# Performance work log

Hardware: AMD Instinct MI355X
Metric: run time of the kernel (lower is better)

## Reference

```python
import jax, jax.numpy as jnp
import numpy as np

N, P, D, C = 8192, 512, 2, 4   # queries, coeff grid points, spatial dim, num coefficients
HA = 32                        # attention_net hidden
HP, CP = 32, 16                # pointswise_mlp hidden / output
HG = 256                       # green_function_net hidden


def setup_inputs() -> dict:
    key = jax.random.key(0)
    ks = jax.random.split(key, 16)
    g = lambda k, shp, s: jax.random.normal(k, shp, dtype=jnp.float32) * s
    return {
        "r": g(ks[0], (N, 2 * D), 1.0),
        "r_prime": g(ks[1], (N, 2 * D), 1.0),
        "coeff_x": g(ks[2], (P, D), 1.0),
        "coeff_y": g(ks[3], (P, C), 1.0),
        # attention_net MLP (no bias): concat(q,k)=4 -> 32 -> 32 -> 1
        "Wa1": g(ks[4], (2 * D, HA), 0.5),
        "Wa2": g(ks[5], (HA, HA), 1.0 / np.sqrt(HA)),
        "Wa3": g(ks[6], (HA, 1), 1.0 / np.sqrt(HA)),
        # pointswise_mlp: C -> 32 -> 16
        "Wp1": g(ks[7], (C, HP), 0.5), "bp1": jnp.zeros((HP,), jnp.float32),
        "Wp2": g(ks[8], (HP, CP), 1.0 / np.sqrt(HP)), "bp2": jnp.zeros((CP,), jnp.float32),
        # green_function_net: 4+4+16=24 -> 256 -> 256 -> 1 (exp at the end)
        "Wg1": g(ks[9], (2 * D + 2 * D + CP, HG), 1.0 / np.sqrt(24.0)), "bg1": jnp.zeros((HG,), jnp.float32),
        "Wg2": g(ks[10], (HG, HG), 1.0 / np.sqrt(HG)), "bg2": jnp.zeros((HG,), jnp.float32),
        "Wg3": g(ks[11], (HG, 1), 0.1 / np.sqrt(HG)), "bg3": jnp.zeros((1,), jnp.float32),
    }


def reference(r, r_prime, coeff_x, coeff_y,
              Wa1, Wa2, Wa3, Wp1, bp1, Wp2, bp2,
              Wg1, bg1, Wg2, bg2, Wg3, bg3):
    # --- CoefficientNet: pairwise MLP attention over the coefficient grid ---
    q = r[:, :D]  # (N, 2) spatial position only
    # first layer of attn MLP on concat([q, k]) split into q- and k- parts
    h = jax.nn.relu(q @ Wa1[:D][None if False else slice(None)]  # (N, HA)
                    [..., :] [..., :]  # no-op for readability
                    if False else (q @ Wa1[:D])[:, None, :] + (coeff_x @ Wa1[D:])[None, :, :])  # (N, P, HA)
    h = jax.nn.relu(h @ Wa2)                     # (N, P, HA)
    logits = (h @ Wa3)[..., 0]                   # (N, P)
    attn = jax.nn.softmax(logits, axis=-1)       # (N, P)
    attn_out = attn @ coeff_y                    # (N, C)
    c = jax.nn.relu(attn_out @ Wp1 + bp1) @ Wp2 + bp2  # (N, CP)
    # --- GreenFunctionNet ---
    x = jnp.concatenate([r, r_prime, c], axis=-1)       # (N, 24)
    g1 = jax.nn.relu(x @ Wg1 + bg1)
    g2 = jax.nn.relu(g1 @ Wg2 + bg2)
    return jnp.exp(g2 @ Wg3 + bg3)                      # (N, 1)
```

## Files before the change

kernel.cpp:

```cpp
#include <hip/hip_runtime.h>
#include <math.h>

#define N_ 8192
#define P_ 512

typedef __fp16 half8  __attribute__((ext_vector_type(8)));
typedef __fp16 half2t __attribute__((ext_vector_type(2)));
typedef float  floatx16 __attribute__((ext_vector_type(16)));

union H8 { half8 v; half2t h2[4]; };

static __device__ __forceinline__ half2t pk2(float a, float b) {
    return __builtin_amdgcn_cvt_pkrtz(a, b);
}

#define HP_OFF 17408
#define XS_OFF 21760

__global__ __launch_bounds__(512, 4) void k_fused(
    const float* __restrict__ r,
    const float* __restrict__ rp,
    const float* __restrict__ coeff_x,
    const float* __restrict__ coeff_y,
    const float* __restrict__ Wa1,
    const float* __restrict__ Wa2,
    const float* __restrict__ Wa3,
    const float* __restrict__ Wp1,
    const float* __restrict__ bp1,
    const float* __restrict__ Wp2,
    const float* __restrict__ bp2,
    const float* __restrict__ Wg1,
    const float* __restrict__ bg1,
    const float* __restrict__ Wg2,
    const float* __restrict__ bg2,
    const float* __restrict__ Wg3,
    const float* __restrict__ bg3,
    float* __restrict__ out)
{
    __shared__ __align__(16) unsigned char reg0[49152];
    __shared__ __align__(16) float4 cyS[512];
    __shared__ float sA[8][32];
    __shared__ float aoA[4][8][32];
    __shared__ float aoS[32][4];

    const int tid  = threadIdx.x;
    const int n0   = blockIdx.x * 32;
    const int lane = tid & 63;
    const int wv   = tid >> 6;
    const int j32  = lane & 31;
    const int hl   = lane >> 5;
    const int k0g  = hl * 8;

    {
        const float2 cx = ((const float2*)coeff_x)[tid];
        half2t* wrow = (half2t*)(reg0 + tid * 96);
#pragma unroll
        for (int q = 0; q < 16; ++q) {
            const float b0 = cx.x * Wa1[64 + 2*q]     + cx.y * Wa1[96 + 2*q];
            const float b1 = cx.x * Wa1[64 + 2*q + 1] + cx.y * Wa1[96 + 2*q + 1];
            wrow[q] = pk2(b0, b1);
        }
        cyS[tid] = ((const float4*)coeff_y)[tid];
    }

    H8 anh1, anh2;
    {
        const float2 rv = ((const float2*)r)[2 * (n0 + j32)];
#pragma unroll
        for (int q = 0; q < 4; ++q) {
            const int k1 = k0g + 2*q, k2 = 16 + k0g + 2*q;
            anh1.h2[q] = pk2(rv.x*Wa1[k1]   + rv.y*Wa1[32+k1],
                             rv.x*Wa1[k1+1] + rv.y*Wa1[32+k1+1]);
            anh2.h2[q] = pk2(rv.x*Wa1[k2]   + rv.y*Wa1[32+k2],
                             rv.x*Wa1[k2+1] + rv.y*Wa1[32+k2+1]);
        }
    }
    H8 af1, af2;
#pragma unroll
    for (int q = 0; q < 4; ++q) {
        af1.h2[q] = pk2(Wa2[(k0g + 2*q)     * 32 + j32],
                        Wa2[(k0g + 2*q + 1) * 32 + j32]);
        af2.h2[q] = pk2(Wa2[(16 + k0g + 2*q)     * 32 + j32],
                        Wa2[(16 + k0g + 2*q + 1) * 32 + j32]);
    }
    half2t w3h[8];
#pragma unroll
    for (int q = 0; q < 8; ++q) {
        const int r0 = ((2*q) & 3) + 8*(q >> 1) + 4*hl;
        w3h[q] = pk2(Wa3[r0], Wa3[r0 + 1]);
    }

    __syncthreads();

    const half2t zero2 = pk2(0.f, 0.f);
    float s = 0.0f, aox = 0.f, aoy = 0.f, aoz = 0.f, aow = 0.f;

#pragma unroll 2
    for (int pl = 0; pl < 64; ++pl) {
        const int ploc = wv * 64 + pl;
        const half2t* rowq = (const half2t*)(reg0 + ploc * 96) + hl * 4;

        H8 bf1, bf2;
#pragma unroll
        for (int q = 0; q < 4; ++q) {
            bf1.h2[q] = __builtin_elementwise_max(anh1.h2[q] + rowq[q],     zero2);
            bf2.h2[q] = __builtin_elementwise_max(anh2.h2[q] + rowq[8 + q], zero2);
        }

        floatx16 zc = {};
        floatx16 acc = __builtin_amdgcn_mfma_f32_32x32x16_f16(af1.v, bf1.v, zc, 0, 0, 0);
        acc = __builtin_amdgcn_mfma_f32_32x32x16_f16(af2.v, bf2.v, acc, 0, 0, 0);

        float d0, d1, d2, d3;
        {
            half2t z0 = __builtin_elementwise_max(pk2(acc[0],  acc[1]),  zero2);
            half2t z1 = __builtin_elementwise_max(pk2(acc[2],  acc[3]),  zero2);
            half2t z2 = __builtin_elementwise_max(pk2(acc[4],  acc[5]),  zero2);
            half2t z3 = __builtin_elementwise_max(pk2(acc[6],  acc[7]),  zero2);
            half2t z4 = __builtin_elementwise_max(pk2(acc[8],  acc[9]),  zero2);
            half2t z5 = __builtin_elementwise_max(pk2(acc[10], acc[11]), zero2);
            half2t z6 = __builtin_elementwise_max(pk2(acc[12], acc[13]), zero2);
            half2t z7 = __builtin_elementwise_max(pk2(acc[14], acc[15]), zero2);
            d0 = __builtin_amdgcn_fdot2(z1, w3h[1], __builtin_amdgcn_fdot2(z0, w3h[0], 0.f, false), false);
            d1 = __builtin_amdgcn_fdot2(z3, w3h[3], __builtin_amdgcn_fdot2(z2, w3h[2], 0.f, false), false);
            d2 = __builtin_amdgcn_fdot2(z5, w3h[5], __builtin_amdgcn_fdot2(z4, w3h[4], 0.f, false), false);
            d3 = __builtin_amdgcn_fdot2(z7, w3h[7], __builtin_amdgcn_fdot2(z6, w3h[6], 0.f, false), false);
        }
        float dot = (d0 + d1) + (d2 + d3);
        dot += __shfl_xor(dot, 32);

        const float e = __expf(dot);
        const float4 cyv = cyS[ploc];
        s   += e;
        aox += e * cyv.x;
        aoy += e * cyv.y;
        aoz += e * cyv.z;
        aow += e * cyv.w;
    }

    const int jcol = (wv << 5) + j32;
    const int nB = tid & 31;
    const int iB = tid >> 5;

    float wg2p[32];
#pragma unroll
    for (int q = 0; q < 4; ++q)
#pragma unroll
        for (int t = 0; t < 4; ++t) {
            const int kb = q*16 + hl*8 + 2*t;
            wg2p[q*8 + 2*t]     = Wg2[kb*256 + jcol];
            wg2p[q*8 + 2*t + 1] = Wg2[(kb+1)*256 + jcol];
        }
    float wg1f[8], wg1g[8];
    const float bg1v = bg1[jcol];
#pragma unroll
    for (int q = 0; q < 4; ++q) {
        wg1f[2*q]   = Wg1[(k0g + 2*q)*256 + jcol];
        wg1f[2*q+1] = Wg1[(k0g + 2*q + 1)*256 + jcol];
        wg1g[2*q]   = Wg1[(16 + 2*q)*256 + jcol];
        wg1g[2*q+1] = Wg1[(17 + 2*q)*256 + jcol];
    }
    float xpre = 0.f;
    if (tid < 256) {
        const int nn = tid >> 3, k = tid & 7;
        xpre = (k < 4) ? r[(n0+nn)*4 + k] : rp[(n0+nn)*4 + k - 4];
    }
    float wpb[2], wpA[2][4];
#pragma unroll
    for (int rep = 0; rep < 2; ++rep) {
        const int i = iB + rep*16;
        wpb[rep]    = bp1[i];
        wpA[rep][0] = Wp1[i];
        wpA[rep][1] = Wp1[32 + i];
        wpA[rep][2] = Wp1[64 + i];
        wpA[rep][3] = Wp1[96 + i];
    }
    const float bp2v = bp2[iB];
    const float bg2v = bg2[jcol];
    const float w3vv = Wg3[jcol];
    const float bg3v = bg3[0];

    if (lane < 32) {
        sA[wv][lane]      = s;
        aoA[0][wv][lane]  = aox;
        aoA[1][wv][lane]  = aoy;
        aoA[2][wv][lane]  = aoz;
        aoA[3][wv][lane]  = aow;
    }
    __syncthreads();

    if (tid < 32) {
        float S = 0.f, A0 = 0.f, A1 = 0.f, A2 = 0.f, A3 = 0.f;
#pragma unroll
        for (int w = 0; w < 8; ++w) {
            S  += sA[w][tid];
            A0 += aoA[0][w][tid];
            A1 += aoA[1][w][tid];
            A2 += aoA[2][w][tid];
            A3 += aoA[3][w][tid];
        }
        const float inv = 1.0f / S;
        aoS[tid][0] = A0 * inv;
        aoS[tid][1] = A1 * inv;
        aoS[tid][2] = A2 * inv;
        aoS[tid][3] = A3 * inv;
    }
    __syncthreads();

    float* hpS = (float*)(reg0 + HP_OFF);
    float* xS  = (float*)(reg0 + XS_OFF);

    if (tid < 256) {
        const int nn = tid >> 3, k = tid & 7;
        xS[nn*25 + k] = xpre;
    }
    {
        const float a0 = aoS[nB][0], a1 = aoS[nB][1], a2 = aoS[nB][2], a3 = aoS[nB][3];
#pragma unroll
        for (int rep = 0; rep < 2; ++rep) {
            const int i = iB + rep*16;
            float a = wpb[rep] + a0*wpA[rep][0] + a1*wpA[rep][1]
                               + a2*wpA[rep][2] + a3*wpA[rep][3];
            hpS[nB*33 + i] = fmaxf(a, 0.0f);
        }
    }
    __syncthreads();

    {
        float a = bp2v;
#pragma unroll
        for (int i = 0; i < 32; ++i) a += hpS[nB*33 + i] * Wp2[i*16 + iB];
        xS[nB*25 + 8 + iB] = a;
    }
    __syncthreads();

    __fp16* g1S = (__fp16*)reg0;

    {
        H8 xa1, xa2, wb1, wb2;
        const float* xrow = xS + j32 * 25;
#pragma unroll
        for (int q = 0; q < 4; ++q) {
            xa1.h2[q] = pk2(xrow[k0g + 2*q], xrow[k0g + 2*q + 1]);
            wb1.h2[q] = pk2(wg1f[2*q], wg1f[2*q+1]);
            if (hl == 0) {
                xa2.h2[q] = pk2(xrow[16 + 2*q], xrow[16 + 2*q + 1]);
                wb2.h2[q] = pk2(wg1g[2*q], wg1g[2*q+1]);
            } else {
                xa2.h2[q] = pk2(0.f, 0.f);
                wb2.h2[q] = pk2(0.f, 0.f);
            }
        }
        floatx16 g1acc = {};
        g1acc = __builtin_amdgcn_mfma_f32_32x32x16_f16(xa1.v, wb1.v, g1acc, 0, 0, 0);
        g1acc = __builtin_amdgcn_mfma_f32_32x32x16_f16(xa2.v, wb2.v, g1acc, 0, 0, 0);

#pragma unroll
        for (int i = 0; i < 16; ++i) {
            const int row = (i & 3) + 8*(i >> 2) + 4*hl;
            g1S[row*264 + jcol] = (__fp16)fmaxf(g1acc[i] + bg1v, 0.0f);
        }
    }
    __syncthreads();

    {
        floatx16 acc2 = {};
        const __fp16* arow = g1S + j32 * 264;

        H8 wB[4], wBn[4];
#pragma unroll
        for (int q = 0; q < 4; ++q)
#pragma unroll
            for (int t = 0; t < 4; ++t)
                wB[q].h2[t] = pk2(wg2p[q*8 + 2*t], wg2p[q*8 + 2*t + 1]);

#pragma unroll
        for (int c = 0; c < 4; ++c) {
            if (c < 3) {
#pragma unroll
                for (int q = 0; q < 4; ++q) {
                    const int kb = (c*4 + 4 + q)*16 + hl*8;
#pragma unroll
                    for (int t = 0; t < 4; ++t)
                        wBn[q].h2[t] = pk2(Wg2[(kb + 2*t)*256 + jcol],
                                           Wg2[(kb + 2*t + 1)*256 + jcol]);
                }
            }
#pragma unroll
            for (int q = 0; q < 4; ++q) {
                H8 af;
                af.v = *(const half8*)(arow + (c*4 + q)*16 + hl*8);
                acc2 = __builtin_amdgcn_mfma_f32_32x32x16_f16(af.v, wB[q].v, acc2, 0, 0, 0);
            }
#pragma unroll
            for (int q = 0; q < 4; ++q) wB[q] = wBn[q];
        }

        float part[16];
#pragma unroll
        for (int i = 0; i < 16; ++i)
            part[i] = fmaxf(acc2[i] + bg2v, 0.0f) * w3vv;
#pragma unroll
        for (int off = 1; off <= 16; off <<= 1) {
#pragma unroll
            for (int i = 0; i < 16; ++i) part[i] += __shfl_xor(part[i], off);
        }
        float* redS = &sA[0][0];
        if ((lane & 31) == 0) {
#pragma unroll
            for (int i = 0; i < 16; ++i) {
                const int row = (i & 3) + 8*(i >> 2) + 4*hl;
                redS[wv*32 + row] = part[i];
            }
        }
        __syncthreads();

        if (tid < 32) {
            float v = bg3v;
#pragma unroll
            for (int w = 0; w < 8; ++w) v += redS[w*32 + tid];
            out[n0 + tid] = __expf(v);
        }
    }
}

extern "C" void kernel_launch(void* const* d_in, const int* in_sizes, int n_in,
                              void* d_out, int out_size, void* d_ws, size_t ws_size,
                              hipStream_t stream)
{
    const float* r   = (const float*)d_in[0];
    const float* rp  = (const float*)d_in[1];
    const float* cx  = (const float*)d_in[2];
    const float* cy  = (const float*)d_in[3];
    const float* Wa1 = (const float*)d_in[4];
    const float* Wa2 = (const float*)d_in[5];
    const float* Wa3 = (const float*)d_in[6];
    const float* Wp1 = (const float*)d_in[7];
    const float* bp1 = (const float*)d_in[8];
    const float* Wp2 = (const float*)d_in[9];
    const float* bp2 = (const float*)d_in[10];
    const float* Wg1 = (const float*)d_in[11];
    const float* bg1 = (const float*)d_in[12];
    const float* Wg2 = (const float*)d_in[13];
    const float* bg2 = (const float*)d_in[14];
    const float* Wg3 = (const float*)d_in[15];
    const float* bg3 = (const float*)d_in[16];

    hipLaunchKernelGGL(k_fused, dim3(N_/32), dim3(512), 0, stream,
                       r, rp, cx, cy, Wa1, Wa2, Wa3, Wp1, bp1, Wp2, bp2,
                       Wg1, bg1, Wg2, bg2, Wg3, bg3, (float*)d_out);
}
```

Before: 109.5 us.

## Prefetch more Wg2 weights earlier and parallelise softmax reduction across threads

Loads the first half of the Wg2 weight slice (64 floats) before the softmax barrier and packs it and the Wg1 operands to fp16 ahead of time. The remaining Wg2 quarters are issued as global loads two MFMA groups ahead. The tail also stages Wp2 in shared memory, spreads the 8-wave softmax sum reduction over 160 threads, and moves the normalisation into the pointwise MLP. The aim is to hide global-load latency in the epilogue, at the cost of higher register pressure under the 512x4 launch bound, which may cause spills.

```diff
diff --git a/kernel.cpp b/kernel.cpp
--- a/kernel.cpp
+++ b/kernel.cpp
@@ -14,8 +14,9 @@
     return __builtin_amdgcn_cvt_pkrtz(a, b);
 }
 
-#define HP_OFF 17408
-#define XS_OFF 21760
+#define HP_OFF  17408
+#define XS_OFF  21760
+#define WP2_OFF 25088
 
 __global__ __launch_bounds__(512, 4) void k_fused(
     const float* __restrict__ r,
@@ -42,6 +43,7 @@
     __shared__ float sA[8][32];
     __shared__ float aoA[4][8][32];
     __shared__ float aoS[32][4];
+    __shared__ float sredS[32];
 
     const int tid  = threadIdx.x;
     const int n0   = blockIdx.x * 32;
@@ -142,14 +144,14 @@
     const int nB = tid & 31;
     const int iB = tid >> 5;
 
-    float wg2p[32];
-#pragma unroll
-    for (int q = 0; q < 4; ++q)
+    float wg2f[64];
+#pragma unroll
+    for (int kk = 0; kk < 8; ++kk)
 #pragma unroll
         for (int t = 0; t < 4; ++t) {
-            const int kb = q*16 + hl*8 + 2*t;
-            wg2p[q*8 + 2*t]     = Wg2[kb*256 + jcol];
-            wg2p[q*8 + 2*t + 1] = Wg2[(kb+1)*256 + jcol];
+            const int kb = kk*16 + hl*8 + 2*t;
+            wg2f[kk*8 + 2*t]     = Wg2[kb*256 + jcol];
+            wg2f[kk*8 + 2*t + 1] = Wg2[(kb+1)*256 + jcol];
         }
     float wg1f[8], wg1g[8];
     const float bg1v = bg1[jcol];
@@ -160,6 +162,7 @@
         wg1g[2*q]   = Wg1[(16 + 2*q)*256 + jcol];
         wg1g[2*q+1] = Wg1[(17 + 2*q)*256 + jcol];
     }
+    const float wp2pre = Wp2[tid];
     float xpre = 0.f;
     if (tid < 256) {
         const int nn = tid >> 3, k = tid & 7;
@@ -180,6 +183,19 @@
     const float w3vv = Wg3[jcol];
     const float bg3v = bg3[0];
 
+    H8 wPre[8];
+#pragma unroll
+    for (int kk = 0; kk < 8; ++kk)
+#pragma unroll
+        for (int t = 0; t < 4; ++t)
+            wPre[kk].h2[t] = pk2(wg2f[kk*8 + 2*t], wg2f[kk*8 + 2*t + 1]);
+    H8 wb1p, wb2p;
+#pragma unroll
+    for (int q = 0; q < 4; ++q) {
+        wb1p.h2[q] = pk2(wg1f[2*q], wg1f[2*q+1]);
+        wb2p.h2[q] = (hl == 0) ? pk2(wg1g[2*q], wg1g[2*q+1]) : pk2(0.f, 0.f);
+    }
+
     if (lane < 32) {
         sA[wv][lane]      = s;
         aoA[0][wv][lane]  = aox;
@@ -189,21 +205,21 @@
     }
     __syncthreads();
 
-    if (tid < 32) {
-        float S = 0.f, A0 = 0.f, A1 = 0.f, A2 = 0.f, A3 = 0.f;
-#pragma unroll
-        for (int w = 0; w < 8; ++w) {
-            S  += sA[w][tid];
-            A0 += aoA[0][w][tid];
-            A1 += aoA[1][w][tid];
-            A2 += aoA[2][w][tid];
-            A3 += aoA[3][w][tid];
-        }
-        const float inv = 1.0f / S;
-        aoS[tid][0] = A0 * inv;
-        aoS[tid][1] = A1 * inv;
-        aoS[tid][2] = A2 * inv;
-        aoS[tid][3] = A3 * inv;
+    float* wp2S = (float*)(reg0 + WP2_OFF);
+    wp2S[tid] = wp2pre;
+    if (tid < 160) {
+        const int g5 = tid >> 5, c = tid & 31;
+        if (g5 == 0) {
+            float S = 0.f;
+#pragma unroll
+            for (int w = 0; w < 8; ++w) S += sA[w][c];
+            sredS[c] = S;
+        } else {
+            float A = 0.f;
+#pragma unroll
+            for (int w = 0; w < 8; ++w) A += aoA[g5-1][w][c];
+            aoS[c][g5-1] = A;
+        }
     }
     __syncthreads();
 
@@ -215,13 +231,14 @@
         xS[nn*25 + k] = xpre;
     }
     {
+        const float inv = 1.0f / sredS[nB];
         const float a0 = aoS[nB][0], a1 = aoS[nB][1], a2 = aoS[nB][2], a3 = aoS[nB][3];
 #pragma unroll
         for (int rep = 0; rep < 2; ++rep) {
-            const int i = iB + rep*16;
-            float a = wpb[rep] + a0*wpA[rep][0] + a1*wpA[rep][1]
-                               + a2*wpA[rep][2] + a3*wpA[rep][3];
-            hpS[nB*33 + i] = fmaxf(a, 0.0f);
+            float t = a0*wpA[rep][0] + a1*wpA[rep][1]
+                    + a2*wpA[rep][2] + a3*wpA[rep][3];
+            float a = wpb[rep] + inv * t;
+            hpS[nB*33 + iB + rep*16] = fmaxf(a, 0.0f);
         }
     }
     __syncthreads();
@@ -229,7 +246,7 @@
     {
         float a = bp2v;
 #pragma unroll
-        for (int i = 0; i < 32; ++i) a += hpS[nB*33 + i] * Wp2[i*16 + iB];
+        for (int i = 0; i < 32; ++i) a += hpS[nB*33 + i] * wp2S[i*16 + iB];
         xS[nB*25 + 8 + iB] = a;
     }
     __syncthreads();
@@ -237,23 +254,17 @@
     __fp16* g1S = (__fp16*)reg0;
 
     {
-        H8 xa1, xa2, wb1, wb2;
+        H8 xa1, xa2;
         const float* xrow = xS + j32 * 25;
 #pragma unroll
         for (int q = 0; q < 4; ++q) {
             xa1.h2[q] = pk2(xrow[k0g + 2*q], xrow[k0g + 2*q + 1]);
-            wb1.h2[q] = pk2(wg1f[2*q], wg1f[2*q+1]);
-            if (hl == 0) {
-                xa2.h2[q] = pk2(xrow[16 + 2*q], xrow[16 + 2*q + 1]);
-                wb2.h2[q] = pk2(wg1g[2*q], wg1g[2*q+1]);
-            } else {
-                xa2.h2[q] = pk2(0.f, 0.f);
-                wb2.h2[q] = pk2(0.f, 0.f);
-            }
+            xa2.h2[q] = (hl == 0) ? pk2(xrow[16 + 2*q], xrow[16 + 2*q + 1])
+                                  : pk2(0.f, 0.f);
         }
         floatx16 g1acc = {};
-        g1acc = __builtin_amdgcn_mfma_f32_32x32x16_f16(xa1.v, wb1.v, g1acc, 0, 0, 0);
-        g1acc = __builtin_amdgcn_mfma_f32_32x32x16_f16(xa2.v, wb2.v, g1acc, 0, 0, 0);
+        g1acc = __builtin_amdgcn_mfma_f32_32x32x16_f16(xa1.v, wb1p.v, g1acc, 0, 0, 0);
+        g1acc = __builtin_amdgcn_mfma_f32_32x32x16_f16(xa2.v, wb2p.v, g1acc, 0, 0, 0);
 
 #pragma unroll
         for (int i = 0; i < 16; ++i) {
@@ -267,33 +278,62 @@
         floatx16 acc2 = {};
         const __fp16* arow = g1S + j32 * 264;
 
-        H8 wB[4], wBn[4];
+        float l2[32];
 #pragma unroll
         for (int q = 0; q < 4; ++q)
 #pragma unroll
+            for (int t = 0; t < 4; ++t) {
+                const int kb = (8 + q)*16 + hl*8 + 2*t;
+                l2[q*8 + 2*t]     = Wg2[kb*256 + jcol];
+                l2[q*8 + 2*t + 1] = Wg2[(kb+1)*256 + jcol];
+            }
+#pragma unroll
+        for (int q = 0; q < 4; ++q) {
+            H8 af;
+            af.v = *(const half8*)(arow + q*16 + hl*8);
+            acc2 = __builtin_amdgcn_mfma_f32_32x32x16_f16(af.v, wPre[q].v, acc2, 0, 0, 0);
+        }
+
+        float l3[32];
+#pragma unroll
+        for (int q = 0; q < 4; ++q)
+#pragma unroll
+            for (int t = 0; t < 4; ++t) {
+                const int kb = (12 + q)*16 + hl*8 + 2*t;
+                l3[q*8 + 2*t]     = Wg2[kb*256 + jcol];
+                l3[q*8 + 2*t + 1] = Wg2[(kb+1)*256 + jcol];
+            }
+#pragma unroll
+        for (int q = 0; q < 4; ++q) {
+            H8 af;
+            af.v = *(const half8*)(arow + (4 + q)*16 + hl*8);
+            acc2 = __builtin_amdgcn_mfma_f32_32x32x16_f16(af.v, wPre[4+q].v, acc2, 0, 0, 0);
+        }
+
+        H8 w2[4];
+#pragma unroll
+        for (int q = 0; q < 4; ++q)
+#pragma unroll
             for (int t = 0; t < 4; ++t)
-                wB[q].h2[t] = pk2(wg2p[q*8 + 2*t], wg2p[q*8 + 2*t + 1]);
-
-#pragma unroll
-        for (int c = 0; c < 4; ++c) {
-            if (c < 3) {
-#pragma unroll
-                for (int q = 0; q < 4; ++q) {
-                    const int kb = (c*4 + 4 + q)*16 + hl*8;
-#pragma unroll
-                    for (int t = 0; t < 4; ++t)
-                        wBn[q].h2[t] = pk2(Wg2[(kb + 2*t)*256 + jcol],
-                                           Wg2[(kb + 2*t + 1)*256 + jcol]);
-                }
-            }
-#pragma unroll
-            for (int q = 0; q < 4; ++q) {
-                H8 af;
-                af.v = *(const half8*)(arow + (c*4 + q)*16 + hl*8);
-                acc2 = __builtin_amdgcn_mfma_f32_32x32x16_f16(af.v, wB[q].v, acc2, 0, 0, 0);
-            }
-#pragma unroll
-            for (int q = 0; q < 4; ++q) wB[q] = wBn[q];
+                w2[q].h2[t] = pk2(l2[q*8 + 2*t], l2[q*8 + 2*t + 1]);
+#pragma unroll
+        for (int q = 0; q < 4; ++q) {
+            H8 af;
+            af.v = *(const half8*)(arow + (8 + q)*16 + hl*8);
+            acc2 = __builtin_amdgcn_mfma_f32_32x32x16_f16(af.v, w2[q].v, acc2, 0, 0, 0);
+        }
+
+        H8 w3[4];
+#pragma unroll
+        for (int q = 0; q < 4; ++q)
+#pragma unroll
+            for (int t = 0; t < 4; ++t)
+                w3[q].h2[t] = pk2(l3[q*8 + 2*t], l3[q*8 + 2*t + 1]);
+#pragma unroll
+        for (int q = 0; q < 4; ++q) {
+            H8 af;
+            af.v = *(const half8*)(arow + (12 + q)*16 + hl*8);
+            acc2 = __builtin_amdgcn_mfma_f32_32x32x16_f16(af.v, w3[q].v, acc2, 0, 0, 0);
         }
 
         float part[16];
```

Result: slower. 126.4 us (+15.4%).
